# Kernel optimization log

Hardware: AMD Instinct MI355X
Metric: run time of the kernel (lower is better)

Reference implementation:

```python
import jax, jax.numpy as jnp
import numpy as np


def _knn_idx(xyz, kk):
    # faithful to knn_point: full pairwise squared L2, topk of -dist
    diff = xyz[:, None, :, :] - xyz[:, :, None, :]      # (B, Nq, Nd, 3)
    dist = jnp.sum(diff * diff, axis=-1)                # (B, Nq, Nd)
    _, idx = jax.lax.top_k(-dist, kk)                   # (B, Nq, kk)
    return idx


def setup_inputs() -> dict:
    key = jax.random.key(0)
    k1, k2, k3, k4 = jax.random.split(key, 4)
    B, N, C = 4, 4096, 64
    return {
        "xyz": jax.random.normal(k1, (B, N, 3), dtype=jnp.float32),
        "w1": jax.random.normal(k2, (C, 3), dtype=jnp.float32) * 0.1,
        "w2": jax.random.normal(k3, (C, C), dtype=jnp.float32) * 0.1,
        "w3": jax.random.normal(k4, (C, C), dtype=jnp.float32) * 0.1,
        "k": 16,
    }


def reference(xyz, w1, w2, w3, k):
    # group(xyz, None, k): knn with k+1 neighbors, drop self (index 0)
    idx = _knn_idx(xyz, k + 1)[:, :, 1:]                # (B, N, k)
    # gather neighbor coords per batch: (B, N, k, 3)
    grouped = jax.vmap(lambda pts, i: pts[i])(xyz, idx)
    grouped = grouped - xyz[:, :, None, :]              # relative coords
    x = jnp.transpose(grouped, (0, 3, 1, 2))            # (B, 3, N, k)
    # 1x1 conv stack (bias=False) as einsum contractions over channel dim
    x = jax.nn.relu(jnp.einsum("oc,bcnk->bonk", w1, x))
    x = jax.nn.relu(jnp.einsum("oc,bcnk->bonk", w2, x))
    x = jnp.einsum("oc,bcnk->bonk", w3, x)
    # max-pool over neighbor axis -> (B, C, N)
    return jnp.max(x, axis=3)
```

## Files before the change

kernel.cpp:

```cpp
#include <hip/hip_runtime.h>
#include <hip/hip_bf16.h>

#define NPTS  4096
#define BATCH 4
#define KK    16
#define CH    64
#define SURV_CAP 40

typedef __attribute__((ext_vector_type(8))) short bf16x8;
typedef __attribute__((ext_vector_type(4))) float f32x4;

__device__ __forceinline__ unsigned short bhi(float x) {
    return (unsigned short)(__float_as_uint(x) >> 16);
}
__device__ __forceinline__ unsigned short blo(float x) {
    const float h = __uint_as_float(__float_as_uint(x) & 0xffff0000u);
    return (unsigned short)(__float_as_uint(x - h) >> 16);
}
__device__ __forceinline__ unsigned pk2(unsigned short a, unsigned short b) {
    return (unsigned)a | ((unsigned)b << 16);
}

__device__ __forceinline__ float ref_dist(float px, float py, float pz,
                                          float qx, float qy, float qz) {
#pragma clang fp contract(off)
    const float dx = px - qx, dy = py - qy, dz = pz - qz;
    const float sx = dx * dx, sy = dy * dy, sz = dz * dz;
    return (sx + sy) + sz;
}

__global__ __launch_bounds__(512, 4) void knn_kernel(const float* __restrict__ xyz,
                                                     int* __restrict__ knn_idx) {
    __shared__ float2 sXY[NPTS];
    __shared__ float  sZ[NPTS];
    __shared__ int sidx[8][4][SURV_CAP];
    __shared__ int scnt[8][4];
    const int wave = threadIdx.x >> 6;
    const int lane = threadIdx.x & 63;
    const int q0 = blockIdx.x * 32 + wave * 4;
    const int b = q0 >> 12;
    const int i0 = q0 & (NPTS - 1);
    const float* xb = xyz + (size_t)b * NPTS * 3;

#pragma unroll
    for (int r = 0; r < NPTS / 512; ++r) {
        const int pt = r * 512 + threadIdx.x;
        sXY[pt] = make_float2(xb[pt * 3 + 0], xb[pt * 3 + 1]);
        sZ[pt] = xb[pt * 3 + 2];
    }
    if (lane < 4) scnt[wave][lane] = 0;
    __syncthreads();

    float qx[4], qy[4], qz[4], ax[4], ay[4], az[4];
#pragma unroll
    for (int v = 0; v < 4; ++v) {
        const float2 t = sXY[i0 + v];
        qx[v] = t.x; qy[v] = t.y; qz[v] = sZ[i0 + v];
        ax[v] = -2.f * qx[v]; ay[v] = -2.f * qy[v]; az[v] = -2.f * qz[v];
    }

    float mn[4] = {3.4e38f, 3.4e38f, 3.4e38f, 3.4e38f};
#pragma unroll 8
    for (int t = 0; t < 64; ++t) {
        const float2 pxy = sXY[t * 64 + lane];
        const float pz = sZ[t * 64 + lane];
        const float px = pxy.x, py = pxy.y;
        const float w = fmaf(px, px, fmaf(py, py, pz * pz));
#pragma unroll
        for (int v = 0; v < 4; ++v) {
            const float s = fmaf(pz, az[v], fmaf(py, ay[v], fmaf(px, ax[v], w)));
            mn[v] = fminf(mn[v], s);
        }
    }

#pragma unroll
    for (int k = 2; k <= 64; k <<= 1) {
#pragma unroll
        for (int jj = k >> 1; jj > 0; jj >>= 1) {
            const bool tm = (((lane & jj) == 0) == ((lane & k) == 0));
#pragma unroll
            for (int v = 0; v < 4; ++v) {
                const float p = __shfl_xor(mn[v], jj);
                mn[v] = ((p < mn[v]) == tm) ? p : mn[v];
            }
        }
    }
    float T[4];
#pragma unroll
    for (int v = 0; v < 4; ++v) T[v] = __shfl(mn[v], 16) + 1e-3f;

#pragma unroll 4
    for (int t = 0; t < 64; ++t) {
        const float2 pxy = sXY[t * 64 + lane];
        const float pz = sZ[t * 64 + lane];
        const float px = pxy.x, py = pxy.y;
        const float w = fmaf(px, px, fmaf(py, py, pz * pz));
#pragma unroll
        for (int v = 0; v < 4; ++v) {
            const float s = fmaf(pz, az[v], fmaf(py, ay[v], fmaf(px, ax[v], w)));
            if (s <= T[v]) {
                const int slot = atomicAdd(&scnt[wave][v], 1);
                if (slot < SURV_CAP) sidx[wave][v][slot] = t * 64 + lane;
            }
        }
    }
    int cnt[4];
#pragma unroll
    for (int v = 0; v < 4; ++v) cnt[v] = scnt[wave][v];

    unsigned long long key[4];
#pragma unroll
    for (int v = 0; v < 4; ++v) {
        key[v] = ~0ull;
        if (lane < cnt[v] && cnt[v] <= SURV_CAP) {
            const int j = sidx[wave][v][lane];
            const float2 pxy = sXY[j];
            const float d = ref_dist(pxy.x, pxy.y, sZ[j], qx[v], qy[v], qz[v]);
            key[v] = ((unsigned long long)__float_as_uint(d) << 32) | (unsigned)j;
        }
    }

#pragma unroll
    for (int k = 2; k <= 64; k <<= 1) {
#pragma unroll
        for (int jj = k >> 1; jj > 0; jj >>= 1) {
            const bool tm = (((lane & jj) == 0) == ((lane & k) == 0));
#pragma unroll
            for (int v = 0; v < 4; ++v) {
                const unsigned long long p = __shfl_xor(key[v], jj);
                key[v] = ((p < key[v]) == tm) ? p : key[v];
            }
        }
    }

    auto fallback = [&](int q, float fqx, float fqy, float fqz) {
        float dp = -1.0f; int jp = -1;
        for (int pass = 0; pass < KK + 1; ++pass) {
            float dmin = 3.4e38f; int jmin = 0x7fffffff;
            for (int t = 0; t < 64; ++t) {
                const int j = t * 64 + lane;
                const float2 pxy = sXY[j];
                const float d = ref_dist(pxy.x, pxy.y, sZ[j], fqx, fqy, fqz);
                const bool valid = (d > dp) || (d == dp && j > jp);
                const bool less = valid && (d < dmin || (d == dmin && j < jmin));
                dmin = less ? d : dmin;
                jmin = less ? j : jmin;
            }
#pragma unroll
            for (int off = 32; off > 0; off >>= 1) {
                const float d2 = __shfl_xor(dmin, off);
                const int   j2 = __shfl_xor(jmin, off);
                if (d2 < dmin || (d2 == dmin && j2 < jmin)) { dmin = d2; jmin = j2; }
            }
            if (pass >= 1 && lane == 0) knn_idx[(size_t)q * KK + pass - 1] = jmin;
            dp = dmin; jp = jmin;
        }
    };

#pragma unroll
    for (int v = 0; v < 4; ++v) {
        if (cnt[v] <= SURV_CAP) {
            if (lane >= 1 && lane <= KK)
                knn_idx[(size_t)(q0 + v) * KK + lane - 1] = (int)(key[v] & 0xffffffffu);
        } else fallback(q0 + v, qx[v], qy[v], qz[v]);
    }
}

__global__ __launch_bounds__(256, 2) void mlp_kernel(const float* __restrict__ xyz,
                                                     const int* __restrict__ knn_idx,
                                                     const float* __restrict__ w1,
                                                     const float* __restrict__ w2,
                                                     const float* __restrict__ w3,
                                                     float* __restrict__ out) {
    __shared__ __align__(16) unsigned short w2h[64 * 64], w2l[64 * 64];
    __shared__ __align__(16) unsigned short w3h[64 * 64], w3l[64 * 64];
    __shared__ __align__(16) unsigned short cbh[4][32 * 64], cbl[4][32 * 64];
    __shared__ __align__(16) float obuf[CH][36];

    const int tid = threadIdx.x;
    const int wave = tid >> 6, lane = tid & 63;
    const int lq = lane & 15, lg = lane >> 4;
    const int bx = blockIdx.x;
    const int bb = bx >> 7;
    const int nbase = (bx & 127) * 32;
    const float* xb = xyz + (size_t)bb * NPTS * 3;

    {
        const int r = tid >> 2, kb = (tid & 3) * 16;
#pragma unroll
        for (int kp = 0; kp < 16; kp += 2) {
            const int k = kb + kp;
            const float a0 = w2[r * 64 + k], a1 = w2[r * 64 + k + 1];
            const float c0 = w3[r * 64 + k], c1 = w3[r * 64 + k + 1];
            const int byt = r * 128 + (((k >> 3) ^ (r & 7)) << 4) + (k & 7) * 2;
            *(unsigned*)((char*)w2h + byt) = pk2(bhi(a0), bhi(a1));
            *(unsigned*)((char*)w2l + byt) = pk2(blo(a0), blo(a1));
            *(unsigned*)((char*)w3h + byt) = pk2(bhi(c0), bhi(c1));
            *(unsigned*)((char*)w3l + byt) = pk2(blo(c0), blo(c1));
        }
    }

    float w1v[2][8][3];
#pragma unroll
    for (int s = 0; s < 2; ++s)
#pragma unroll
        for (int j = 0; j < 8; ++j) {
            const int k = s * 32 + lg * 8 + j;
#pragma unroll
            for (int c = 0; c < 3; ++c) w1v[s][j][c] = w1[k * 3 + c];
        }

    const int col = lane & 31;
    float gxa[4], gya[4], gza[4];
#pragma unroll
    for (int g = 0; g < 4; ++g) {
        const int n = nbase + g * 8 + wave * 2 + (col >> 4);
        const int j = knn_idx[((size_t)bb * NPTS + n) * KK + (col & 15)];
        gxa[g] = xb[j * 3 + 0] - xb[n * 3 + 0];
        gya[g] = xb[j * 3 + 1] - xb[n * 3 + 1];
        gza[g] = xb[j * 3 + 2] - xb[n * 3 + 2];
    }
    __syncthreads();

    unsigned short* const cbH = cbh[wave];
    unsigned short* const cbL = cbl[wave];

#pragma unroll
    for (int g = 0; g < 4; ++g) {
        bf16x8 b1h[2][2], b1l[2][2];
#pragma unroll
        for (int t = 0; t < 2; ++t) {
            const int src = t * 16 + lq;
            const float sgx = __shfl(gxa[g], src);
            const float sgy = __shfl(gya[g], src);
            const float sgz = __shfl(gza[g], src);
#pragma unroll
            for (int s = 0; s < 2; ++s) {
                bf16x8 hh, ll;
#pragma unroll
                for (int j = 0; j < 8; ++j) {
                    float v = fmaf(w1v[s][j][2], sgz,
                              fmaf(w1v[s][j][1], sgy, w1v[s][j][0] * sgx));
                    v = fmaxf(v, 0.f);
                    hh[j] = (short)bhi(v);
                    ll[j] = (short)blo(v);
                }
                b1h[s][t] = hh; b1l[s][t] = ll;
            }
        }

        f32x4 acc[4][2];
#pragma unroll
        for (int m = 0; m < 4; ++m)
#pragma unroll
            for (int t = 0; t < 2; ++t) acc[m][t] = (f32x4){0.f, 0.f, 0.f, 0.f};
#pragma unroll
        for (int m = 0; m < 4; ++m) {
            const int r = m * 16 + lq;
#pragma unroll
            for (int s = 0; s < 2; ++s) {
                const int byt = r * 128 + (((s * 4 + lg) ^ (r & 7)) << 4);
                const bf16x8 ah = *(const bf16x8*)((const char*)w2h + byt);
                const bf16x8 al = *(const bf16x8*)((const char*)w2l + byt);
#pragma unroll
                for (int t = 0; t < 2; ++t) {
                    acc[m][t] = __builtin_amdgcn_mfma_f32_16x16x32_bf16(ah, b1h[s][t], acc[m][t], 0, 0, 0);
                    acc[m][t] = __builtin_amdgcn_mfma_f32_16x16x32_bf16(ah, b1l[s][t], acc[m][t], 0, 0, 0);
                    acc[m][t] = __builtin_amdgcn_mfma_f32_16x16x32_bf16(al, b1h[s][t], acc[m][t], 0, 0, 0);
                }
            }
        }

#pragma unroll
        for (int m = 0; m < 4; ++m)
#pragma unroll
            for (int t = 0; t < 2; ++t) {
                f32x4 v = acc[m][t];
#pragma unroll
                for (int e = 0; e < 4; ++e) v[e] = fmaxf(v[e], 0.f);
                const int co = t * 16 + lq;
                const int k0 = m * 16 + lg * 4;
                const int byt = co * 128 + (((k0 >> 3) ^ (co & 7)) << 4) + (k0 & 7) * 2;
                uint2 hw, lw;
                hw.x = pk2(bhi(v[0]), bhi(v[1])); hw.y = pk2(bhi(v[2]), bhi(v[3]));
                lw.x = pk2(blo(v[0]), blo(v[1])); lw.y = pk2(blo(v[2]), blo(v[3]));
                *(uint2*)((char*)cbH + byt) = hw;
                *(uint2*)((char*)cbL + byt) = lw;
            }

        bf16x8 xh[2][2], xl[2][2];
#pragma unroll
        for (int s = 0; s < 2; ++s)
#pragma unroll
            for (int t = 0; t < 2; ++t) {
                const int co = t * 16 + lq;
                const int byt = co * 128 + (((s * 4 + lg) ^ (co & 7)) << 4);
                xh[s][t] = *(const bf16x8*)((const char*)cbH + byt);
                xl[s][t] = *(const bf16x8*)((const char*)cbL + byt);
            }
        f32x4 acc3[4][2];
#pragma unroll
        for (int mb = 0; mb < 4; ++mb)
#pragma unroll
            for (int t = 0; t < 2; ++t) acc3[mb][t] = (f32x4){0.f, 0.f, 0.f, 0.f};
#pragma unroll
        for (int mb = 0; mb < 4; ++mb) {
            const int r = mb * 16 + lq;
#pragma unroll
            for (int s = 0; s < 2; ++s) {
                const int byt = r * 128 + (((s * 4 + lg) ^ (r & 7)) << 4);
                const bf16x8 wh = *(const bf16x8*)((const char*)w3h + byt);
                const bf16x8 wl = *(const bf16x8*)((const char*)w3l + byt);
#pragma unroll
                for (int t = 0; t < 2; ++t) {
                    acc3[mb][t] = __builtin_amdgcn_mfma_f32_16x16x32_bf16(xh[s][t], wh, acc3[mb][t], 0, 0, 0);
                    acc3[mb][t] = __builtin_amdgcn_mfma_f32_16x16x32_bf16(xh[s][t], wl, acc3[mb][t], 0, 0, 0);
                    acc3[mb][t] = __builtin_amdgcn_mfma_f32_16x16x32_bf16(xl[s][t], wh, acc3[mb][t], 0, 0, 0);
                }
            }
        }

#pragma unroll
        for (int mb = 0; mb < 4; ++mb)
#pragma unroll
            for (int t = 0; t < 2; ++t) {
                float v = fmaxf(fmaxf(acc3[mb][t][0], acc3[mb][t][1]),
                                fmaxf(acc3[mb][t][2], acc3[mb][t][3]));
                v = fmaxf(v, __shfl_xor(v, 16));
                v = fmaxf(v, __shfl_xor(v, 32));
                if (lg == 0) obuf[mb * 16 + lq][g * 8 + wave * 2 + t] = v;
            }
    }
    __syncthreads();

    {
        const int c = tid >> 2, seg = tid & 3;
        const float4 v0 = *(const float4*)&obuf[c][seg * 8];
        const float4 v1 = *(const float4*)&obuf[c][seg * 8 + 4];
        float* op = &out[((size_t)(bb * CH + c)) * NPTS + nbase + seg * 8];
        *(float4*)op = v0;
        *(float4*)(op + 4) = v1;
    }
}

extern "C" void kernel_launch(void* const* d_in, const int* in_sizes, int n_in,
                              void* d_out, int out_size, void* d_ws, size_t ws_size,
                              hipStream_t stream) {
    (void)in_sizes; (void)n_in; (void)out_size; (void)ws_size;
    const float* xyz = (const float*)d_in[0];
    const float* w1  = (const float*)d_in[1];
    const float* w2  = (const float*)d_in[2];
    const float* w3  = (const float*)d_in[3];
    int*   knn = (int*)d_ws;
    float* out = (float*)d_out;

    knn_kernel<<<BATCH * NPTS / 32, 512, 0, stream>>>(xyz, knn);
    mlp_kernel<<<BATCH * NPTS / 32, 256, 0, stream>>>(xyz, knn, w1, w2, w3, out);
}
```

Measured before the change: 106.6 us.

## Reduce MLP split-bf16 precision and halve points per block

The MLP kernel drops most of the split hi/lo bf16 emulation. Weights w2 and w3 are stored as single round-to-nearest bf16, layer 2 keeps two MFMAs per step (hi and lo activations) instead of three, and layer 3 uses one MFMA per step with single-bf16 activations and weights. Each block now handles 16 points instead of 32, with twice as many blocks and a launch-bounds occupancy hint of 3, and shared memory shrinks. This cuts MFMA work and LDS traffic but lowers accuracy to roughly bf16 level, which may break the tolerance.

Result: faster. 103.4 us (-3.1%).

```diff
diff --git a/kernel.cpp b/kernel.cpp
--- a/kernel.cpp
+++ b/kernel.cpp
@@ -16,6 +16,10 @@
 __device__ __forceinline__ unsigned short blo(float x) {
     const float h = __uint_as_float(__float_as_uint(x) & 0xffff0000u);
     return (unsigned short)(__float_as_uint(x - h) >> 16);
+}
+__device__ __forceinline__ unsigned short brn(float x) {
+    const unsigned u = __float_as_uint(x);
+    return (unsigned short)((u + 0x7fffu + ((u >> 16) & 1u)) >> 16);
 }
 __device__ __forceinline__ unsigned pk2(unsigned short a, unsigned short b) {
     return (unsigned)a | ((unsigned)b << 16);
@@ -166,23 +170,23 @@
     }
 }
 
-__global__ __launch_bounds__(256, 2) void mlp_kernel(const float* __restrict__ xyz,
+__global__ __launch_bounds__(256, 3) void mlp_kernel(const float* __restrict__ xyz,
                                                      const int* __restrict__ knn_idx,
                                                      const float* __restrict__ w1,
                                                      const float* __restrict__ w2,
                                                      const float* __restrict__ w3,
                                                      float* __restrict__ out) {
-    __shared__ __align__(16) unsigned short w2h[64 * 64], w2l[64 * 64];
-    __shared__ __align__(16) unsigned short w3h[64 * 64], w3l[64 * 64];
-    __shared__ __align__(16) unsigned short cbh[4][32 * 64], cbl[4][32 * 64];
-    __shared__ __align__(16) float obuf[CH][36];
+    __shared__ __align__(16) unsigned short w2b[64 * 64];
+    __shared__ __align__(16) unsigned short w3b[64 * 64];
+    __shared__ __align__(16) unsigned short cb[4][32 * 64];
+    __shared__ __align__(16) float obuf[CH][20];
 
     const int tid = threadIdx.x;
     const int wave = tid >> 6, lane = tid & 63;
     const int lq = lane & 15, lg = lane >> 4;
     const int bx = blockIdx.x;
-    const int bb = bx >> 7;
-    const int nbase = (bx & 127) * 32;
+    const int bb = bx >> 8;
+    const int nbase = (bx & 255) * 16;
     const float* xb = xyz + (size_t)bb * NPTS * 3;
 
     {
@@ -190,13 +194,9 @@
 #pragma unroll
         for (int kp = 0; kp < 16; kp += 2) {
             const int k = kb + kp;
-            const float a0 = w2[r * 64 + k], a1 = w2[r * 64 + k + 1];
-            const float c0 = w3[r * 64 + k], c1 = w3[r * 64 + k + 1];
             const int byt = r * 128 + (((k >> 3) ^ (r & 7)) << 4) + (k & 7) * 2;
-            *(unsigned*)((char*)w2h + byt) = pk2(bhi(a0), bhi(a1));
-            *(unsigned*)((char*)w2l + byt) = pk2(blo(a0), blo(a1));
-            *(unsigned*)((char*)w3h + byt) = pk2(bhi(c0), bhi(c1));
-            *(unsigned*)((char*)w3l + byt) = pk2(blo(c0), blo(c1));
+            *(unsigned*)((char*)w2b + byt) = pk2(brn(w2[r * 64 + k]), brn(w2[r * 64 + k + 1]));
+            *(unsigned*)((char*)w3b + byt) = pk2(brn(w3[r * 64 + k]), brn(w3[r * 64 + k + 1]));
         }
     }
 
@@ -211,9 +211,9 @@
         }
 
     const int col = lane & 31;
-    float gxa[4], gya[4], gza[4];
-#pragma unroll
-    for (int g = 0; g < 4; ++g) {
+    float gxa[2], gya[2], gza[2];
+#pragma unroll
+    for (int g = 0; g < 2; ++g) {
         const int n = nbase + g * 8 + wave * 2 + (col >> 4);
         const int j = knn_idx[((size_t)bb * NPTS + n) * KK + (col & 15)];
         gxa[g] = xb[j * 3 + 0] - xb[n * 3 + 0];
@@ -222,11 +222,10 @@
     }
     __syncthreads();
 
-    unsigned short* const cbH = cbh[wave];
-    unsigned short* const cbL = cbl[wave];
-
-#pragma unroll
-    for (int g = 0; g < 4; ++g) {
+    unsigned short* const cbW = cb[wave];
+
+#pragma unroll
+    for (int g = 0; g < 2; ++g) {
         bf16x8 b1h[2][2], b1l[2][2];
 #pragma unroll
         for (int t = 0; t < 2; ++t) {
@@ -260,13 +259,11 @@
 #pragma unroll
             for (int s = 0; s < 2; ++s) {
                 const int byt = r * 128 + (((s * 4 + lg) ^ (r & 7)) << 4);
-                const bf16x8 ah = *(const bf16x8*)((const char*)w2h + byt);
-                const bf16x8 al = *(const bf16x8*)((const char*)w2l + byt);
+                const bf16x8 ah = *(const bf16x8*)((const char*)w2b + byt);
 #pragma unroll
                 for (int t = 0; t < 2; ++t) {
                     acc[m][t] = __builtin_amdgcn_mfma_f32_16x16x32_bf16(ah, b1h[s][t], acc[m][t], 0, 0, 0);
                     acc[m][t] = __builtin_amdgcn_mfma_f32_16x16x32_bf16(ah, b1l[s][t], acc[m][t], 0, 0, 0);
-                    acc[m][t] = __builtin_amdgcn_mfma_f32_16x16x32_bf16(al, b1h[s][t], acc[m][t], 0, 0, 0);
                 }
             }
         }
@@ -281,22 +278,19 @@
                 const int co = t * 16 + lq;
                 const int k0 = m * 16 + lg * 4;
                 const int byt = co * 128 + (((k0 >> 3) ^ (co & 7)) << 4) + (k0 & 7) * 2;
-                uint2 hw, lw;
-                hw.x = pk2(bhi(v[0]), bhi(v[1])); hw.y = pk2(bhi(v[2]), bhi(v[3]));
-                lw.x = pk2(blo(v[0]), blo(v[1])); lw.y = pk2(blo(v[2]), blo(v[3]));
-                *(uint2*)((char*)cbH + byt) = hw;
-                *(uint2*)((char*)cbL + byt) = lw;
-            }
-
-        bf16x8 xh[2][2], xl[2][2];
+                uint2 hw;
+                hw.x = pk2(brn(v[0]), brn(v[1])); hw.y = pk2(brn(v[2]), brn(v[3]));
+                *(uint2*)((char*)cbW + byt) = hw;
+            }
+
+        bf16x8 xh[2][2];
 #pragma unroll
         for (int s = 0; s < 2; ++s)
 #pragma unroll
             for (int t = 0; t < 2; ++t) {
                 const int co = t * 16 + lq;
                 const int byt = co * 128 + (((s * 4 + lg) ^ (co & 7)) << 4);
-                xh[s][t] = *(const bf16x8*)((const char*)cbH + byt);
-                xl[s][t] = *(const bf16x8*)((const char*)cbL + byt);
+                xh[s][t] = *(const bf16x8*)((const char*)cbW + byt);
             }
         f32x4 acc3[4][2];
 #pragma unroll
@@ -309,13 +303,10 @@
 #pragma unroll
             for (int s = 0; s < 2; ++s) {
                 const int byt = r * 128 + (((s * 4 + lg) ^ (r & 7)) << 4);
-                const bf16x8 wh = *(const bf16x8*)((const char*)w3h + byt);
-                const bf16x8 wl = *(const bf16x8*)((const char*)w3l + byt);
+                const bf16x8 wh = *(const bf16x8*)((const char*)w3b + byt);
 #pragma unroll
                 for (int t = 0; t < 2; ++t) {
                     acc3[mb][t] = __builtin_amdgcn_mfma_f32_16x16x32_bf16(xh[s][t], wh, acc3[mb][t], 0, 0, 0);
-                    acc3[mb][t] = __builtin_amdgcn_mfma_f32_16x16x32_bf16(xh[s][t], wl, acc3[mb][t], 0, 0, 0);
-                    acc3[mb][t] = __builtin_amdgcn_mfma_f32_16x16x32_bf16(xl[s][t], wh, acc3[mb][t], 0, 0, 0);
                 }
             }
         }
@@ -335,11 +326,8 @@
 
     {
         const int c = tid >> 2, seg = tid & 3;
-        const float4 v0 = *(const float4*)&obuf[c][seg * 8];
-        const float4 v1 = *(const float4*)&obuf[c][seg * 8 + 4];
-        float* op = &out[((size_t)(bb * CH + c)) * NPTS + nbase + seg * 8];
-        *(float4*)op = v0;
-        *(float4*)(op + 4) = v1;
+        const float4 v0 = *(const float4*)&obuf[c][seg * 4];
+        *(float4*)&out[((size_t)(bb * CH + c)) * NPTS + nbase + seg * 4] = v0;
     }
 }
 
@@ -355,5 +343,5 @@
     float* out = (float*)d_out;
 
     knn_kernel<<<BATCH * NPTS / 32, 512, 0, stream>>>(xyz, knn);
-    mlp_kernel<<<BATCH * NPTS / 32, 256, 0, stream>>>(xyz, knn, w1, w2, w3, out);
-}
+    mlp_kernel<<<BATCH * NPTS / 16, 256, 0, stream>>>(xyz, knn, w1, w2, w3, out);
+}
```
